# Performance work log

Measured on AMD Instinct MI355X. Metric: run time of the kernel, lower is better.

## Reference

```python
import jax, jax.numpy as jnp
import numpy as np

B, S, T = 256, 512, 20
VOCAB, E, H, SKIP = 100000, 25, 128, 64


def _lstm_scan(x, skip, mask, K, R, Sk, b):
    # x:[S,B,E], skip:[S,B,SKIP], mask:[S,B] bool. Keras RNN mask semantics:
    # masked steps carry previous h/c and emit previous h.
    Bn = x.shape[1]
    Hn = R.shape[0]
    def step(carry, inp):
        h, c = carry
        xt, st, mt = inp
        z = xt @ K + h @ R + st @ Sk + b            # [B,4H]
        zi, zf, zg, zo = jnp.split(z, 4, axis=-1)
        cn = jax.nn.sigmoid(zf) * c + jax.nn.sigmoid(zi) * jnp.tanh(zg)
        hn = jax.nn.sigmoid(zo) * jnp.tanh(cn)
        m = mt[:, None]
        h2 = jnp.where(m, hn, h)
        c2 = jnp.where(m, cn, c)
        return (h2, c2), h2
    init = (jnp.zeros((Bn, Hn), x.dtype), jnp.zeros((Bn, Hn), x.dtype))
    (hF, cF), hs = jax.lax.scan(step, init, (x, skip, mask))
    return hs, hF


def setup_inputs() -> dict:
    key = jax.random.key(0)
    ks = jax.random.split(key, 20)
    p = lambda k, shp: jax.random.normal(k, shp, dtype=jnp.float32) * 0.05
    inp = {
        "input_tags": jax.random.randint(ks[0], (B, S, T), 0, VOCAB, dtype=jnp.int32),
        "embedded_skips": jax.random.normal(ks[1], (B, S, SKIP), dtype=jnp.float32),
        "emb_table": p(ks[2], (VOCAB, E)),
        "kernel_f": p(ks[3], (E, 4 * H)),
        "rec_f": p(ks[4], (H, 4 * H)),
        "skip_f": p(ks[5], (SKIP, 4 * H)),
        "bias_f": jnp.zeros((4 * H,), jnp.float32),
        "kernel_b": p(ks[6], (E, 4 * H)),
        "rec_b": p(ks[7], (H, 4 * H)),
        "skip_b": p(ks[8], (SKIP, 4 * H)),
        "bias_b": jnp.zeros((4 * H,), jnp.float32),
        "Wk": p(ks[9], (2 * H, H)),
        "bk": jnp.zeros((H,), jnp.float32),
        "Wq": p(ks[10], (H, H)),
        "bq": jnp.zeros((H,), jnp.float32),
        "We": p(ks[11], (H, 1)),
        "be": jnp.zeros((1,), jnp.float32),
    }
    return inp


def reference(input_tags, embedded_skips, emb_table,
              kernel_f, rec_f, skip_f, bias_f,
              kernel_b, rec_b, skip_b, bias_b,
              Wk, bk, Wq, bq, We, be):
    mask3 = input_tags != 0                          # [B,S,T]
    emb = emb_table[input_tags]                      # [B,S,T,E]
    num_mask = mask3.astype(emb.dtype)
    summed = jnp.sum(emb * num_mask[..., None], axis=2)   # [B,S,E]
    denom = jnp.sum(num_mask, axis=2)                     # [B,S]
    denom = jnp.where(denom == 0, jnp.ones_like(denom), denom)
    gru_inp = summed / denom[..., None]                   # [B,S,E]
    step_mask = mask3[:, :, 0]                            # [B,S]

    # time-major for scan
    x_t = jnp.swapaxes(gru_inp, 0, 1)
    s_t = jnp.swapaxes(embedded_skips, 0, 1)
    m_t = jnp.swapaxes(step_mask, 0, 1)

    hs_f, h_fwd = _lstm_scan(x_t, s_t, m_t, kernel_f, rec_f, skip_f, bias_f)
    hs_b_rev, _ = _lstm_scan(x_t[::-1], s_t[::-1], m_t[::-1], kernel_b, rec_b, skip_b, bias_b)
    hs_b = hs_b_rev[::-1]
    out = jnp.swapaxes(jnp.concatenate([hs_f, hs_b], axis=-1), 0, 1)  # [B,S,2H]

    keys = out @ Wk + bk                                  # [B,S,H]
    queries = (h_fwd @ Wq + bq)[:, None, :]               # [B,1,H]
    energy = jnp.tanh(keys + queries) @ We + be           # [B,S,1]
    energy = energy + (1.0 - step_mask.astype(energy.dtype))[..., None] * -1e9
    weights = jax.nn.softmax(energy, axis=1)
    context = jnp.sum(weights * out, axis=1)              # [B,2H]
    return context
```

## Files before the change

### kernel.cpp

```cpp
#include <hip/hip_runtime.h>
#include <math.h>

#define Bb 256
#define Ss 512
#define Tt 20
#define Ee 25
#define Hh 128
#define SKIPn 64
#define H4n 512
#define BSn (Bb*Ss)
#define MG 4
#define HP 160
#define ZP 520
#define AP 264
#define LOG2E 1.4426950408889634f

typedef _Float16 f16x8 __attribute__((ext_vector_type(8)));
typedef _Float16 f16x4 __attribute__((ext_vector_type(4)));
typedef float f32x4 __attribute__((ext_vector_type(4)));

__device__ __forceinline__ float rcpf(float x) { return __builtin_amdgcn_rcpf(x); }
__device__ __forceinline__ float exp2f_(float x) { return __builtin_amdgcn_exp2f(x); }

__device__ __forceinline__ void lgkm_barrier() {
    __asm__ __volatile__("" ::: "memory");
    __builtin_amdgcn_s_waitcnt(0xC07F);
    __builtin_amdgcn_s_barrier();
    __asm__ __volatile__("" ::: "memory");
}

__global__ void pool_kernel(const int* __restrict__ tags,
                            const float* __restrict__ table,
                            _Float16* __restrict__ gru16, float* __restrict__ maskf,
                            float* __restrict__ maskt) {
    int group = blockIdx.x * 8 + (threadIdx.x >> 5);
    int lane = threadIdx.x & 31;
    if (group >= BSn) return;
    int b = group >> 9;
    int t = group & (Ss - 1);
    const int* tg = tags + (size_t)group * Tt;
    const int el = (lane < Ee) ? lane : (Ee - 1);

    int tagv[Tt];
#pragma unroll
    for (int tt = 0; tt < Tt; tt++) tagv[tt] = tg[tt];

    float vv[Tt];
#pragma unroll
    for (int tt = 0; tt < Tt; tt++)
        vv[tt] = table[(size_t)tagv[tt] * Ee + el];

    float acc = 0.0f;
    int cnt = 0;
#pragma unroll
    for (int tt = 0; tt < Tt; tt++) {
        const bool nz = (tagv[tt] != 0);
        cnt += nz ? 1 : 0;
        acc += nz ? vv[tt] : 0.0f;
    }
    float scale = rcpf((float)(cnt > 0 ? cnt : 1));
    float v = (lane < Ee) ? acc * scale : 0.0f;
    gru16[((size_t)t * Bb + b) * 32 + lane] = (_Float16)v;
    if (lane == 0) {
        float m = (tagv[0] != 0) ? 1.0f : 0.0f;
        maskf[group] = m;
        maskt[(size_t)t * Bb + b] = m;
    }
}

__global__ void __launch_bounds__(256)
cvt_kernel(const float* __restrict__ in, _Float16* __restrict__ out) {
    size_t i = ((size_t)blockIdx.x * 256 + threadIdx.x) * 8;
    f32x4 a = *(const f32x4*)(in + i);
    f32x4 b = *(const f32x4*)(in + i + 4);
    f16x8 o;
#pragma unroll
    for (int j = 0; j < 4; j++) { o[j] = (_Float16)a[j]; o[j + 4] = (_Float16)b[j]; }
    *(f16x8*)(out + i) = o;
}

__global__ void __launch_bounds__(512)
__attribute__((amdgpu_waves_per_eu(2, 2)))
scan_kernel(const _Float16* __restrict__ gru16, const _Float16* __restrict__ sk16,
            const float* __restrict__ maskt,
            const float* __restrict__ Kf, const float* __restrict__ Rf,
            const float* __restrict__ Skf, const float* __restrict__ bf,
            const float* __restrict__ Kb, const float* __restrict__ Rb,
            const float* __restrict__ Skb, const float* __restrict__ bb,
            _Float16* __restrict__ hs16, float* __restrict__ hfwd)
{
    __shared__ __align__(16) _Float16 h16[2 * MG * HP];
    __shared__ __align__(16) _Float16 zlds[2][16 * 4 * ZP];

    const int tid = threadIdx.x;
    const int lane = tid & 63;
    const int w = tid >> 6;
    const int l16 = lane & 15;
    const int q = lane >> 4;
    const int mb = l16 >> 2;
    const int bg = blockIdx.x & 63;
    const int dir = blockIdx.x >> 6;
    const int b0 = bg * MG;
    const int col = 16 * w + l16;

    const float* Kw = dir ? Kb : Kf;
    const float* Rw = dir ? Rb : Rf;
    const float* Sw = dir ? Skb : Skf;
    const float* bw = dir ? bb : bf;
    const float gs[4] = {LOG2E, LOG2E, 2.0f * LOG2E, LOG2E};

    f16x8 hfr[4][4];
#pragma unroll
    for (int kt = 0; kt < 4; kt++) {
#pragma unroll
        for (int g = 0; g < 4; g++) {
            const int n = g * Hh + col;
            f16x8 v;
#pragma unroll
            for (int j = 0; j < 8; j++)
                v[j] = (_Float16)(Rw[(32 * kt + 8 * q + j) * H4n + n] * gs[g]);
            hfr[kt][g] = v;
        }
    }
    f16x8 bx[4], bs0[4], bs1[4];
    f32x4 biasA[4];
#pragma unroll
    for (int g = 0; g < 4; g++) {
        const int n = g * Hh + col;
        f16x8 vx, v0, v1;
#pragma unroll
        for (int j = 0; j < 8; j++) {
            const int kk = 8 * q + j;
            vx[j] = (_Float16)(((kk < Ee) ? Kw[kk * H4n + n] : 0.0f) * gs[g]);
            v0[j] = (_Float16)(Sw[kk * H4n + n] * gs[g]);
            v1[j] = (_Float16)(Sw[(32 + kk) * H4n + n] * gs[g]);
        }
        bx[g] = vx; bs0[g] = v0; bs1[g] = v1;
        const float bv = bw[g * Hh + col] * gs[g];
        f32x4 ba = {bv, bv, bv, bv};
        biasA[g] = ba;
    }
    const f32x4 zacc4 = {0.0f, 0.0f, 0.0f, 0.0f};

    for (int idx = tid; idx < 2 * MG * HP; idx += 512) h16[idx] = (_Float16)0.0f;

    float c = 0.0f, h = 0.0f;

    const int tsub = l16 >> 2, bbn = l16 & 3;
    const int tg0 = dir ? (Ss - 1 - tsub) : tsub;
    const _Float16* px = gru16 + ((size_t)tg0 * Bb + b0 + bbn) * 32 + 8 * q;
    const _Float16* ps = sk16 + ((size_t)(b0 + bbn) * Ss + tg0) * SKIPn + 8 * q;
    ptrdiff_t pxd = (dir ? -4 : 4) * (ptrdiff_t)(Bb * 32);
    ptrdiff_t psd = (dir ? -4 : 4) * (ptrdiff_t)SKIPn;

    const float* mpf = maskt + (size_t)(dir ? (Ss - 1) : 0) * Bb + b0 + q;
    const ptrdiff_t mdelta = dir ? -(ptrdiff_t)Bb : (ptrdiff_t)Bb;
    float mreg[2];
    mreg[0] = mpf[0]; mreg[1] = mpf[mdelta];
    mpf += 2 * mdelta;

    _Float16* hsp = hs16 + ((size_t)(b0 + q) * Ss + (dir ? Ss - 1 : 0)) * (2 * Hh)
                    + dir * Hh + col;
    const ptrdiff_t odelta = dir ? -(2 * Hh) : (2 * Hh);

    f16x8 gx, g0, g1;
    auto ldA = [&]() {
        gx = *(const f16x8*)px;
        g0 = *(const f16x8*)ps;
        g1 = *(const f16x8*)(ps + 32);
        px += pxd; ps += psd;
    };

    f32x4 zc[4];

    ldA();
#pragma unroll
    for (int T = 0; T < 4; T++) {
        const f16x8 ax = gx, a0 = g0, a1 = g1;
        ldA();
#pragma unroll
        for (int g = 0; g < 4; g++) {
            zc[g] = __builtin_amdgcn_mfma_f32_16x16x32_f16(ax, bx[g],  biasA[g], 0, 0, 0);
            zc[g] = __builtin_amdgcn_mfma_f32_16x16x32_f16(a0, bs0[g], zc[g], 0, 0, 0);
            zc[g] = __builtin_amdgcn_mfma_f32_16x16x32_f16(a1, bs1[g], zc[g], 0, 0, 0);
        }
        _Float16* zw = &zlds[0][0] + ((4 * T + q) * 4) * ZP + col * 4;
#pragma unroll
        for (int r = 0; r < 4; r++) {
            f16x4 o;
            o[0] = (_Float16)zc[0][r]; o[1] = (_Float16)zc[1][r];
            o[2] = (_Float16)zc[2][r]; o[3] = (_Float16)zc[3][r];
            *(f16x4*)(zw + r * ZP) = o;
        }
    }
    __syncthreads();

#pragma unroll 1
    for (int k = 0; k < 32; ++k) {
        const _Float16* zr = &zlds[k & 1][0];
        _Float16* zwb = &zlds[(k + 1) & 1][0];

#pragma unroll
        for (int j = 0; j < 16; ++j) {
            const int T = j >> 2, ph = j & 3;

            const _Float16* hb = h16 + (j & 1) * (MG * HP);
            const f16x8 ah0 = *(const f16x8*)(hb + mb * HP +  0 + 8 * q);
            const f16x8 ah1 = *(const f16x8*)(hb + mb * HP + 32 + 8 * q);
            const f16x8 ah2 = *(const f16x8*)(hb + mb * HP + 64 + 8 * q);
            const f16x8 ah3 = *(const f16x8*)(hb + mb * HP + 96 + 8 * q);
            const f16x4 z4 = *(const f16x4*)(zr + (j * 4 + q) * ZP + col * 4);

            f32x4 accA[4], accB[4];
#pragma unroll
            for (int g = 0; g < 4; g++) {
                accA[g] = __builtin_amdgcn_mfma_f32_16x16x32_f16(ah0, hfr[0][g], zacc4, 0, 0, 0);
                accB[g] = __builtin_amdgcn_mfma_f32_16x16x32_f16(ah1, hfr[1][g], zacc4, 0, 0, 0);
                accA[g] = __builtin_amdgcn_mfma_f32_16x16x32_f16(ah2, hfr[2][g], accA[g], 0, 0, 0);
                accB[g] = __builtin_amdgcn_mfma_f32_16x16x32_f16(ah3, hfr[3][g], accB[g], 0, 0, 0);
            }

            if (ph == 0) {
#pragma unroll
                for (int g = 0; g < 4; g++)
                    zc[g] = __builtin_amdgcn_mfma_f32_16x16x32_f16(gx, bx[g], biasA[g], 0, 0, 0);
            } else if (ph == 1) {
#pragma unroll
                for (int g = 0; g < 4; g++)
                    zc[g] = __builtin_amdgcn_mfma_f32_16x16x32_f16(g0, bs0[g], zc[g], 0, 0, 0);
            } else if (ph == 2) {
#pragma unroll
                for (int g = 0; g < 4; g++)
                    zc[g] = __builtin_amdgcn_mfma_f32_16x16x32_f16(g1, bs1[g], zc[g], 0, 0, 0);
                if (j == 10 && k == 30) { pxd = 0; psd = 0; }
                ldA();
            } else {
                _Float16* zw = zwb + ((4 * T + q) * 4) * ZP + col * 4;
#pragma unroll
                for (int r = 0; r < 4; r++) {
                    f16x4 o;
                    o[0] = (_Float16)zc[0][r]; o[1] = (_Float16)zc[1][r];
                    o[2] = (_Float16)zc[2][r]; o[3] = (_Float16)zc[3][r];
                    *(f16x4*)(zw + r * ZP) = o;
                }
            }

            const float mk = mreg[j & 1];
            mreg[j & 1] = *mpf; mpf += mdelta;
            const float zi = accA[0][0] + accB[0][0] + (float)z4[0];
            const float zf = accA[1][0] + accB[1][0] + (float)z4[1];
            const float zg = accA[2][0] + accB[2][0] + (float)z4[2];
            const float zo = accA[3][0] + accB[3][0] + (float)z4[3];
            const float ei = exp2f_(-zi);
            const float ef = exp2f_(-zf);
            const float eg = exp2f_(-zg);
            const float eo = exp2f_(-zo);
            const float pi = 1.0f + ei, pg = 1.0f + eg, pf = 1.0f + ef;
            const float p  = pi * pg;
            const float t1 = (1.0f - eg) * pf;
            const float cn = fmaf(c, p, t1) * rcpf(pf * p);
            const float ec = exp2f_(cn * (-2.0f * LOG2E));
            const float hn = (1.0f - ec) * rcpf((1.0f + eo) * (1.0f + ec));
            const bool mm = (mk != 0.0f);
            c = mm ? cn : c;
            h = mm ? hn : h;

            _Float16* hw = h16 + ((j + 1) & 1) * (MG * HP);
            hw[q * HP + col] = (_Float16)h;
            *hsp = (_Float16)h;
            hsp += odelta;
            lgkm_barrier();
        }
    }

    if (dir == 0) hfwd[(size_t)(b0 + q) * Hh + col] = h;
}

__global__ void __launch_bounds__(512)
attn_kernel(const _Float16* __restrict__ hs16, const float* __restrict__ hfwd,
            const float* __restrict__ Wq, const float* __restrict__ bq,
            const float* __restrict__ bk,
            const float* __restrict__ Wk, const float* __restrict__ We,
            const float* __restrict__ maskf, float* __restrict__ outp)
{
    __shared__ float hfl[Hh];
    __shared__ float qpart[4][Hh];
    __shared__ float qtot_s[Hh];
    __shared__ float epart[8][Ss];
    __shared__ float ws2[Ss];
    __shared__ float redm[8], reds[8];
    __shared__ float ctxp[16][2 * Hh + 1];
    __shared__ __align__(16) _Float16 atile[2][16 * AP];

    const int tid = threadIdx.x;
    const int lane = tid & 63;
    const int w = tid >> 6;
    const int l16 = lane & 15;
    const int q = lane >> 4;
    const int b = blockIdx.x;
    const int j = 16 * w + l16;

    f16x8 bk16[8];
#pragma unroll
    for (int kt = 0; kt < 8; kt++) {
        f16x8 v;
#pragma unroll
        for (int jj = 0; jj < 8; jj++)
            v[jj] = (_Float16)Wk[(32 * kt + 8 * q + jj) * Hh + j];
        bk16[kt] = v;
    }
    const float wej = We[j];

    if (tid < Hh) hfl[tid] = hfwd[(size_t)b * Hh + tid];
    __syncthreads();
    {
        const int jj = tid & 127, seg = tid >> 7;
        float p = 0.0f;
#pragma unroll
        for (int k = 0; k < 32; k++)
            p += hfl[32 * seg + k] * Wq[(32 * seg + k) * Hh + jj];
        qpart[seg][jj] = p;
    }
    __syncthreads();
    if (tid < Hh)
        qtot_s[tid] = qpart[0][tid] + qpart[1][tid] + qpart[2][tid] + qpart[3][tid]
                      + bq[tid] + bk[tid];
    __syncthreads();
    const float qj = qtot_s[j];

    const _Float16* hb = hs16 + (size_t)b * Ss * (2 * Hh);
    const int srow = tid >> 5;
    const int spart = tid & 31;
    *(f16x8*)(&atile[0][srow * AP + spart * 8]) =
        *(const f16x8*)(hb + (size_t)srow * (2 * Hh) + spart * 8);
    __syncthreads();
#pragma unroll 1
    for (int st = 0; st < 32; st++) {
        const int p = st & 1;
        f16x8 sreg;
        if (st < 31)
            sreg = *(const f16x8*)(hb + (size_t)((st + 1) * 16 + srow) * (2 * Hh) + spart * 8);
        const int s0 = st * 16;
        f32x4 acc = {0.f, 0.f, 0.f, 0.f};
#pragma unroll
        for (int kt = 0; kt < 8; kt++) {
            const f16x8 a = *(const f16x8*)(&atile[p][l16 * AP + kt * 32 + 8 * q]);
            acc = __builtin_amdgcn_mfma_f32_16x16x32_f16(a, bk16[kt], acc, 0, 0, 0);
        }
        float vals[4];
#pragma unroll
        for (int r = 0; r < 4; r++) {
            const float x = acc[r] + qj;
            const float e = exp2f_(fminf(x * (-2.0f * LOG2E), 80.0f));
            vals[r] = (1.0f - e) * rcpf(1.0f + e) * wej;
        }
#pragma unroll
        for (int m = 1; m < 16; m <<= 1) {
#pragma unroll
            for (int r = 0; r < 4; r++) vals[r] += __shfl_xor(vals[r], m);
        }
        if (l16 == 0) {
#pragma unroll
            for (int r = 0; r < 4; r++) epart[w][s0 + 4 * q + r] = vals[r];
        }
        if (st < 31)
            *(f16x8*)(&atile[p ^ 1][srow * AP + spart * 8]) = sreg;
        __syncthreads();
    }

    {
        float e = 0.0f;
#pragma unroll
        for (int ww = 0; ww < 8; ww++) e += epart[ww][tid];
        e += (1.0f - maskf[(size_t)b * Ss + tid]) * -1e9f;
        float mx = e;
#pragma unroll
        for (int off = 32; off > 0; off >>= 1) mx = fmaxf(mx, __shfl_xor(mx, off));
        if (lane == 0) redm[w] = mx;
        __syncthreads();
        mx = redm[0];
#pragma unroll
        for (int ww = 1; ww < 8; ww++) mx = fmaxf(mx, redm[ww]);
        const float p = exp2f_((e - mx) * LOG2E);
        float sm = p;
#pragma unroll
        for (int off = 32; off > 0; off >>= 1) sm += __shfl_xor(sm, off);
        if (lane == 0) reds[w] = sm;
        __syncthreads();
        sm = reds[0] + reds[1] + reds[2] + reds[3] + reds[4] + reds[5] + reds[6] + reds[7];
        ws2[(tid & 31) * 16 + (tid >> 5)] = p * rcpf(sm);
    }
    __syncthreads();

    {
        const int cg = tid & 31;
        const int seg = tid >> 5;
        float a[8];
#pragma unroll
        for (int jj = 0; jj < 8; jj++) a[jj] = 0.0f;
#pragma unroll 4
        for (int sg = 0; sg < 32; sg++) {
            const int s = seg * 32 + sg;
            const float wv = ws2[sg * 16 + seg];
            const f16x8 hv = *(const f16x8*)(hb + (size_t)s * (2 * Hh) + 8 * cg);
#pragma unroll
            for (int jj = 0; jj < 8; jj++) a[jj] = fmaf(wv, (float)hv[jj], a[jj]);
        }
#pragma unroll
        for (int jj = 0; jj < 8; jj++) ctxp[seg][8 * cg + jj] = a[jj];
    }
    __syncthreads();
    if (tid < 2 * Hh) {
        float s = 0.0f;
#pragma unroll
        for (int seg = 0; seg < 16; seg++) s += ctxp[seg][tid];
        outp[(size_t)b * (2 * Hh) + tid] = s;
    }
}

extern "C" void kernel_launch(void* const* d_in, const int* in_sizes, int n_in,
                              void* d_out, int out_size, void* d_ws, size_t ws_size,
                              hipStream_t stream) {
    const int*   tags  = (const int*)d_in[0];
    const float* skips = (const float*)d_in[1];
    const float* table = (const float*)d_in[2];
    const float* Kf    = (const float*)d_in[3];
    const float* Rf    = (const float*)d_in[4];
    const float* Skf   = (const float*)d_in[5];
    const float* bf    = (const float*)d_in[6];
    const float* Kb    = (const float*)d_in[7];
    const float* Rb    = (const float*)d_in[8];
    const float* Skb   = (const float*)d_in[9];
    const float* bb    = (const float*)d_in[10];
    const float* Wk    = (const float*)d_in[11];
    const float* bk    = (const float*)d_in[12];
    const float* Wq    = (const float*)d_in[13];
    const float* bq    = (const float*)d_in[14];
    const float* We    = (const float*)d_in[15];

    char* ws = (char*)d_ws;
    _Float16* gru16 = (_Float16*)ws; ws += (size_t)BSn * 32 * 2;
    _Float16* sk16  = (_Float16*)ws; ws += (size_t)BSn * SKIPn * 2;
    float* maskf = (float*)ws; ws += (size_t)BSn * 4;
    float* maskt_base = (float*)ws; ws += ((size_t)BSn + 4 * Bb) * 4;
    float* maskt = maskt_base + 2 * Bb;
    _Float16* hs16 = (_Float16*)ws; ws += (size_t)BSn * 2 * Hh * 2;
    float* hfwd  = (float*)ws; ws += (size_t)Bb * Hh * 4;

    pool_kernel<<<BSn / 8, 256, 0, stream>>>(tags, table, gru16, maskf, maskt);
    cvt_kernel<<<BSn * SKIPn / (256 * 8), 256, 0, stream>>>(skips, sk16);
    scan_kernel<<<128, 512, 0, stream>>>(gru16, sk16, maskt,
                                         Kf, Rf, Skf, bf,
                                         Kb, Rb, Skb, bb,
                                         hs16, hfwd);
    attn_kernel<<<Bb, 512, 0, stream>>>(hs16, hfwd, Wq, bq, bk, Wk, We, maskf,
                                        (float*)d_out);
}
```

Baseline: 467.3 us.

## Fuse skip conversion into scan and fold softmax-context into attention tile loop

Removes the separate fp32-to-fp16 conversion kernel for skip inputs; the scan kernel now loads fp32 skips directly and converts in registers. The attention kernel drops the global max softmax pass and instead computes unnormalized exp weights per 16-step tile, accumulating the context and the denominator on the fly from the LDS tile already loaded, then normalizes at the end. This avoids a second read of hs16 and one launch, at the cost of extra barriers per tile, double the skip load bytes inside the latency-bound scan, and no max subtraction (it relies on energies being bounded, since tanh output times We is small).

```diff
diff --git a/kernel.cpp b/kernel.cpp
--- a/kernel.cpp
+++ b/kernel.cpp
@@ -68,20 +68,9 @@
     }
 }
 
-__global__ void __launch_bounds__(256)
-cvt_kernel(const float* __restrict__ in, _Float16* __restrict__ out) {
-    size_t i = ((size_t)blockIdx.x * 256 + threadIdx.x) * 8;
-    f32x4 a = *(const f32x4*)(in + i);
-    f32x4 b = *(const f32x4*)(in + i + 4);
-    f16x8 o;
-#pragma unroll
-    for (int j = 0; j < 4; j++) { o[j] = (_Float16)a[j]; o[j + 4] = (_Float16)b[j]; }
-    *(f16x8*)(out + i) = o;
-}
-
 __global__ void __launch_bounds__(512)
 __attribute__((amdgpu_waves_per_eu(2, 2)))
-scan_kernel(const _Float16* __restrict__ gru16, const _Float16* __restrict__ sk16,
+scan_kernel(const _Float16* __restrict__ gru16, const float* __restrict__ skips,
             const float* __restrict__ maskt,
             const float* __restrict__ Kf, const float* __restrict__ Rf,
             const float* __restrict__ Skf, const float* __restrict__ bf,
@@ -149,7 +138,7 @@
     const int tsub = l16 >> 2, bbn = l16 & 3;
     const int tg0 = dir ? (Ss - 1 - tsub) : tsub;
     const _Float16* px = gru16 + ((size_t)tg0 * Bb + b0 + bbn) * 32 + 8 * q;
-    const _Float16* ps = sk16 + ((size_t)(b0 + bbn) * Ss + tg0) * SKIPn + 8 * q;
+    const float*    ps = skips + ((size_t)(b0 + bbn) * Ss + tg0) * SKIPn + 8 * q;
     ptrdiff_t pxd = (dir ? -4 : 4) * (ptrdiff_t)(Bb * 32);
     ptrdiff_t psd = (dir ? -4 : 4) * (ptrdiff_t)SKIPn;
 
@@ -166,8 +155,15 @@
     f16x8 gx, g0, g1;
     auto ldA = [&]() {
         gx = *(const f16x8*)px;
-        g0 = *(const f16x8*)ps;
-        g1 = *(const f16x8*)(ps + 32);
+        const f32x4 u0 = *(const f32x4*)ps;
+        const f32x4 u1 = *(const f32x4*)(ps + 4);
+        const f32x4 u2 = *(const f32x4*)(ps + 32);
+        const f32x4 u3 = *(const f32x4*)(ps + 36);
+#pragma unroll
+        for (int j = 0; j < 4; j++) {
+            g0[j] = (_Float16)u0[j]; g0[j + 4] = (_Float16)u1[j];
+            g1[j] = (_Float16)u2[j]; g1[j + 4] = (_Float16)u3[j];
+        }
         px += pxd; ps += psd;
     };
 
@@ -286,9 +282,10 @@
     __shared__ float hfl[Hh];
     __shared__ float qpart[4][Hh];
     __shared__ float qtot_s[Hh];
-    __shared__ float epart[8][Ss];
-    __shared__ float ws2[Ss];
-    __shared__ float redm[8], reds[8];
+    __shared__ float epart[8][16];
+    __shared__ float psh[16];
+    __shared__ float mls[Ss];
+    __shared__ float dls[16];
     __shared__ float ctxp[16][2 * Hh + 1];
     __shared__ __align__(16) _Float16 atile[2][16 * AP];
 
@@ -299,6 +296,8 @@
     const int q = lane >> 4;
     const int b = blockIdx.x;
     const int j = 16 * w + l16;
+    const int seg = tid >> 5;
+    const int cg = tid & 31;
 
     f16x8 bk16[8];
 #pragma unroll
@@ -311,15 +310,16 @@
     }
     const float wej = We[j];
 
+    mls[tid] = maskf[(size_t)b * Ss + tid];
     if (tid < Hh) hfl[tid] = hfwd[(size_t)b * Hh + tid];
     __syncthreads();
     {
-        const int jj = tid & 127, seg = tid >> 7;
+        const int jj = tid & 127, sg = tid >> 7;
         float p = 0.0f;
 #pragma unroll
         for (int k = 0; k < 32; k++)
-            p += hfl[32 * seg + k] * Wq[(32 * seg + k) * Hh + jj];
-        qpart[seg][jj] = p;
+            p += hfl[32 * sg + k] * Wq[(32 * sg + k) * Hh + jj];
+        qpart[sg][jj] = p;
     }
     __syncthreads();
     if (tid < Hh)
@@ -329,28 +329,36 @@
     const float qj = qtot_s[j];
 
     const _Float16* hb = hs16 + (size_t)b * Ss * (2 * Hh);
-    const int srow = tid >> 5;
-    const int spart = tid & 31;
-    *(f16x8*)(&atile[0][srow * AP + spart * 8]) =
-        *(const f16x8*)(hb + (size_t)srow * (2 * Hh) + spart * 8);
-    __syncthreads();
+    *(f16x8*)(&atile[0][seg * AP + cg * 8]) =
+        *(const f16x8*)(hb + (size_t)seg * (2 * Hh) + cg * 8);
+    float ctxa[8];
+#pragma unroll
+    for (int jj = 0; jj < 8; jj++) ctxa[jj] = 0.0f;
+    float dsum = 0.0f;
+    __syncthreads();
+
 #pragma unroll 1
     for (int st = 0; st < 32; st++) {
         const int p = st & 1;
         f16x8 sreg;
         if (st < 31)
-            sreg = *(const f16x8*)(hb + (size_t)((st + 1) * 16 + srow) * (2 * Hh) + spart * 8);
-        const int s0 = st * 16;
-        f32x4 acc = {0.f, 0.f, 0.f, 0.f};
-#pragma unroll
-        for (int kt = 0; kt < 8; kt++) {
+            sreg = *(const f16x8*)(hb + (size_t)((st + 1) * 16 + seg) * (2 * Hh) + cg * 8);
+
+        f32x4 acc0 = {0.f, 0.f, 0.f, 0.f}, acc1 = {0.f, 0.f, 0.f, 0.f};
+#pragma unroll
+        for (int kt = 0; kt < 4; kt++) {
             const f16x8 a = *(const f16x8*)(&atile[p][l16 * AP + kt * 32 + 8 * q]);
-            acc = __builtin_amdgcn_mfma_f32_16x16x32_f16(a, bk16[kt], acc, 0, 0, 0);
+            acc0 = __builtin_amdgcn_mfma_f32_16x16x32_f16(a, bk16[kt], acc0, 0, 0, 0);
+        }
+#pragma unroll
+        for (int kt = 4; kt < 8; kt++) {
+            const f16x8 a = *(const f16x8*)(&atile[p][l16 * AP + kt * 32 + 8 * q]);
+            acc1 = __builtin_amdgcn_mfma_f32_16x16x32_f16(a, bk16[kt], acc1, 0, 0, 0);
         }
         float vals[4];
 #pragma unroll
         for (int r = 0; r < 4; r++) {
-            const float x = acc[r] + qj;
+            const float x = acc0[r] + acc1[r] + qj;
             const float e = exp2f_(fminf(x * (-2.0f * LOG2E), 80.0f));
             vals[r] = (1.0f - e) * rcpf(1.0f + e) * wej;
         }
@@ -361,60 +369,39 @@
         }
         if (l16 == 0) {
 #pragma unroll
-            for (int r = 0; r < 4; r++) epart[w][s0 + 4 * q + r] = vals[r];
+            for (int r = 0; r < 4; r++) epart[w][4 * q + r] = vals[r];
+        }
+        __syncthreads();
+        if (tid < 16) {
+            float e = epart[0][tid] + epart[1][tid] + epart[2][tid] + epart[3][tid]
+                    + epart[4][tid] + epart[5][tid] + epart[6][tid] + epart[7][tid];
+            psh[tid] = mls[st * 16 + tid] * exp2f_(e * LOG2E);
+        }
+        __syncthreads();
+        {
+            const float wv = psh[seg];
+            const f16x8 hv = *(const f16x8*)(&atile[p][seg * AP + cg * 8]);
+#pragma unroll
+            for (int jj = 0; jj < 8; jj++) ctxa[jj] = fmaf(wv, (float)hv[jj], ctxa[jj]);
+            dsum += wv;
         }
         if (st < 31)
-            *(f16x8*)(&atile[p ^ 1][srow * AP + spart * 8]) = sreg;
+            *(f16x8*)(&atile[p ^ 1][seg * AP + cg * 8]) = sreg;
         __syncthreads();
     }
 
-    {
-        float e = 0.0f;
-#pragma unroll
-        for (int ww = 0; ww < 8; ww++) e += epart[ww][tid];
-        e += (1.0f - maskf[(size_t)b * Ss + tid]) * -1e9f;
-        float mx = e;
-#pragma unroll
-        for (int off = 32; off > 0; off >>= 1) mx = fmaxf(mx, __shfl_xor(mx, off));
-        if (lane == 0) redm[w] = mx;
-        __syncthreads();
-        mx = redm[0];
-#pragma unroll
-        for (int ww = 1; ww < 8; ww++) mx = fmaxf(mx, redm[ww]);
-        const float p = exp2f_((e - mx) * LOG2E);
-        float sm = p;
-#pragma unroll
-        for (int off = 32; off > 0; off >>= 1) sm += __shfl_xor(sm, off);
-        if (lane == 0) reds[w] = sm;
-        __syncthreads();
-        sm = reds[0] + reds[1] + reds[2] + reds[3] + reds[4] + reds[5] + reds[6] + reds[7];
-        ws2[(tid & 31) * 16 + (tid >> 5)] = p * rcpf(sm);
-    }
-    __syncthreads();
-
-    {
-        const int cg = tid & 31;
-        const int seg = tid >> 5;
-        float a[8];
-#pragma unroll
-        for (int jj = 0; jj < 8; jj++) a[jj] = 0.0f;
-#pragma unroll 4
-        for (int sg = 0; sg < 32; sg++) {
-            const int s = seg * 32 + sg;
-            const float wv = ws2[sg * 16 + seg];
-            const f16x8 hv = *(const f16x8*)(hb + (size_t)s * (2 * Hh) + 8 * cg);
-#pragma unroll
-            for (int jj = 0; jj < 8; jj++) a[jj] = fmaf(wv, (float)hv[jj], a[jj]);
-        }
-#pragma unroll
-        for (int jj = 0; jj < 8; jj++) ctxp[seg][8 * cg + jj] = a[jj];
-    }
+#pragma unroll
+    for (int jj = 0; jj < 8; jj++) ctxp[seg][8 * cg + jj] = ctxa[jj];
+    if (cg == 0) dls[seg] = dsum;
     __syncthreads();
     if (tid < 2 * Hh) {
         float s = 0.0f;
 #pragma unroll
-        for (int seg = 0; seg < 16; seg++) s += ctxp[seg][tid];
-        outp[(size_t)b * (2 * Hh) + tid] = s;
+        for (int sg = 0; sg < 16; sg++) s += ctxp[sg][tid];
+        float d = 0.0f;
+#pragma unroll
+        for (int sg = 0; sg < 16; sg++) d += dls[sg];
+        outp[(size_t)b * (2 * Hh) + tid] = s * rcpf(d);
     }
 }
 
@@ -440,7 +427,6 @@
 
     char* ws = (char*)d_ws;
     _Float16* gru16 = (_Float16*)ws; ws += (size_t)BSn * 32 * 2;
-    _Float16* sk16  = (_Float16*)ws; ws += (size_t)BSn * SKIPn * 2;
     float* maskf = (float*)ws; ws += (size_t)BSn * 4;
     float* maskt_base = (float*)ws; ws += ((size_t)BSn + 4 * Bb) * 4;
     float* maskt = maskt_base + 2 * Bb;
@@ -448,8 +434,7 @@
     float* hfwd  = (float*)ws; ws += (size_t)Bb * Hh * 4;
 
     pool_kernel<<<BSn / 8, 256, 0, stream>>>(tags, table, gru16, maskf, maskt);
-    cvt_kernel<<<BSn * SKIPn / (256 * 8), 256, 0, stream>>>(skips, sk16);
-    scan_kernel<<<128, 512, 0, stream>>>(gru16, sk16, maskt,
+    scan_kernel<<<128, 512, 0, stream>>>(gru16, skips, maskt,
                                          Kf, Rf, Skf, bf,
                                          Kb, Rb, Skb, bb,
                                          hs16, hfwd);
```

After: 562.1 us. +20.3%, slower.
